# Kernel optimization log

Hardware: AMD Instinct MI355X
Metric: run time of the kernel (lower is better)

The kernel has to match this reference:

```python
import jax, jax.numpy as jnp
import numpy as np

# Fixed inverse-Haar 2x2 filters (spatial only; depth kernel size is 1)
K_LL = jnp.array([[0.5, 0.5], [0.5, 0.5]], dtype=jnp.float32)
K_LH = jnp.array([[-0.5, 0.5], [-0.5, 0.5]], dtype=jnp.float32)
K_HL = jnp.array([[-0.5, -0.5], [0.5, 0.5]], dtype=jnp.float32)
K_HH = jnp.array([[0.5, -0.5], [-0.5, 0.5]], dtype=jnp.float32)


def _upsample2x(v, k):
    # conv_transpose3d with single-channel 1x2x2 kernel, stride (1,2,2):
    # out[b,d,2i+p,2j+q] = v[b,d,i,j] * k[p,q]
    b, d, h, w = v.shape
    o = jnp.einsum('bdhw,pq->bdhpwq', v, k)
    return o.reshape(b, d, 2 * h, 2 * w)


def setup_inputs() -> dict:
    key = jax.random.key(0)
    k1, k2, k3 = jax.random.split(key, 3)
    B, D, H, W = 8, 32, 128, 128
    x_LL = jax.random.normal(k1, (B, D, H, W), dtype=jnp.float32)
    x = jax.random.normal(k2, (B, 4, D, H, W), dtype=jnp.float32)
    y = jax.random.normal(k3, (B, D, 2 * H, 2 * W), dtype=jnp.float32)
    return {"x_LL": x_LL, "x": x, "y": y}


def reference(x_LL, x, y):
    LL = _upsample2x(x_LL, K_LL)
    LH = _upsample2x(x[:, 1], K_LH)
    HL = _upsample2x(x[:, 2], K_HL)
    HH = _upsample2x(x[:, 3], K_HH)
    return jnp.concatenate((LL, LH, HL, HH, y), axis=1)
```

## Files before the change

kernel.cpp:

```cpp
#include <hip/hip_runtime.h>


#define BB 8
#define DD 32
#define HH_IN 128
#define WW_IN 128
#define H2 256
#define W2 256
#define C_OUT 160
#define W4 64

__global__ __launch_bounds__(256) void haar_iwt_cat_kernel(
    const float* __restrict__ xLL,
    const float* __restrict__ x,
    const float* __restrict__ y,
    float*       __restrict__ out,
    long long total4)
{
    const long long stride = (long long)gridDim.x * blockDim.x;
    for (long long idx = (long long)blockIdx.x * blockDim.x + threadIdx.x;
         idx < total4; idx += stride) {
        const int w4       = (int)(idx & (W4 - 1));
        const long long t1 = idx >> 6;
        const int h2       = (int)(t1 & (H2 - 1));
        const long long bc = t1 >> 8;
        const int c        = (int)(bc % C_OUT);
        const int b        = (int)(bc / C_OUT);

        float4 o;
        if (c >= 128) {
            const int d = c - 128;
            const float4* src = (const float4*)(
                y + ((((long long)b * DD + d) * H2 + h2) * (long long)W2));
            o = src[w4];
        } else {
            const int sel = c >> 5;
            const int d   = c & 31;
            const int h   = h2 >> 1;
            const int p   = h2 & 1;
            const float* src;
            if (sel == 0) {
                src = xLL + ((((long long)b * DD + d) * HH_IN + h) * (long long)WW_IN);
            } else {
                src = x + (((((long long)b * 4 + sel) * DD + d) * HH_IN + h) * (long long)WW_IN);
            }
            const float2 v = ((const float2*)src)[w4];
            float k0, k1;
            switch (sel) {
                case 0:  k0 =  0.5f;              k1 =  0.5f; break;
                case 1:  k0 = -0.5f;              k1 =  0.5f; break;
                case 2:  k0 = p ?  0.5f : -0.5f;  k1 =  k0;   break;
                default: k0 = p ? -0.5f :  0.5f;  k1 = -k0;   break;
            }
            o.x = v.x * k0;
            o.y = v.x * k1;
            o.z = v.y * k0;
            o.w = v.y * k1;
        }
        ((float4*)out)[idx] = o;
    }
}

extern "C" void kernel_launch(void* const* d_in, const int* in_sizes, int n_in,
                              void* d_out, int out_size, void* d_ws, size_t ws_size,
                              hipStream_t stream) {
    const float* xLL = (const float*)d_in[0];
    const float* x   = (const float*)d_in[1];
    const float* y   = (const float*)d_in[2];
    float*       out = (float*)d_out;

    const long long total4 = (long long)BB * C_OUT * H2 * W4;
    const int block = 256;
    const int grid  = 2048;

    haar_iwt_cat_kernel<<<grid, block, 0, stream>>>(xLL, x, y, out, total4);
}
```

Measured before the change: 94.95 us.

## Map each wavefront to one input row, emitting two output rows with nontemporal accesses

After: 85.95 us. 1.1x faster.

```diff
diff --git a/kernel.cpp b/kernel.cpp
--- a/kernel.cpp
+++ b/kernel.cpp
@@ -1,64 +1,63 @@
 #include <hip/hip_runtime.h>
 
 
-#define BB 8
 #define DD 32
-#define HH_IN 128
-#define WW_IN 128
+#define H_IN 128
+#define W_IN 128
 #define H2 256
 #define W2 256
-#define C_OUT 160
-#define W4 64
+
+typedef float f32x4 __attribute__((ext_vector_type(4)));
+typedef float f32x2 __attribute__((ext_vector_type(2)));
 
 __global__ __launch_bounds__(256) void haar_iwt_cat_kernel(
     const float* __restrict__ xLL,
     const float* __restrict__ x,
     const float* __restrict__ y,
-    float*       __restrict__ out,
-    long long total4)
+    float*       __restrict__ out)
 {
-    const long long stride = (long long)gridDim.x * blockDim.x;
-    for (long long idx = (long long)blockIdx.x * blockDim.x + threadIdx.x;
-         idx < total4; idx += stride) {
-        const int w4       = (int)(idx & (W4 - 1));
-        const long long t1 = idx >> 6;
-        const int h2       = (int)(t1 & (H2 - 1));
-        const long long bc = t1 >> 8;
-        const int c        = (int)(bc % C_OUT);
-        const int b        = (int)(bc / C_OUT);
+    const unsigned tid  = threadIdx.x;
+    const unsigned lane = tid & 63u;
+    const unsigned u = blockIdx.x * 4u + (tid >> 6);
 
-        float4 o;
-        if (c >= 128) {
-            const int d = c - 128;
-            const float4* src = (const float4*)(
-                y + ((((long long)b * DD + d) * H2 + h2) * (long long)W2));
-            o = src[w4];
-        } else {
-            const int sel = c >> 5;
-            const int d   = c & 31;
-            const int h   = h2 >> 1;
-            const int p   = h2 & 1;
-            const float* src;
-            if (sel == 0) {
-                src = xLL + ((((long long)b * DD + d) * HH_IN + h) * (long long)WW_IN);
-            } else {
-                src = x + (((((long long)b * 4 + sel) * DD + d) * HH_IN + h) * (long long)WW_IN);
-            }
-            const float2 v = ((const float2*)src)[w4];
-            float k0, k1;
-            switch (sel) {
-                case 0:  k0 =  0.5f;              k1 =  0.5f; break;
-                case 1:  k0 = -0.5f;              k1 =  0.5f; break;
-                case 2:  k0 = p ?  0.5f : -0.5f;  k1 =  k0;   break;
-                default: k0 = p ? -0.5f :  0.5f;  k1 = -k0;   break;
-            }
-            o.x = v.x * k0;
-            o.y = v.x * k1;
-            o.z = v.y * k0;
-            o.w = v.y * k1;
-        }
-        ((float4*)out)[idx] = o;
+    const unsigned i = u & (H_IN - 1u);
+    unsigned t = u >> 7;
+    const unsigned d = t & (DD - 1u);
+    t >>= 5;
+    const unsigned b   = t / 5u;
+    const unsigned sel = t - b * 5u;
+
+    float* orow = out + (((size_t)(b * 160u + sel * 32u + d) * H2 + 2u * i) * W2);
+    f32x4* o0 = ((f32x4*)orow) + lane;
+    f32x4* o1 = ((f32x4*)(orow + W2)) + lane;
+
+    if (sel == 4u) {
+        const float* yrow = y + (((size_t)(b * DD + d) * H2 + 2u * i) * W2);
+        const f32x4 v0 = __builtin_nontemporal_load(((const f32x4*)yrow) + lane);
+        const f32x4 v1 = __builtin_nontemporal_load(((const f32x4*)(yrow + W2)) + lane);
+        __builtin_nontemporal_store(v0, o0);
+        __builtin_nontemporal_store(v1, o1);
+        return;
     }
+
+    const float* src = (sel == 0u)
+        ? xLL + ((size_t)(b * DD + d) * H_IN + i) * W_IN
+        : x   + ((size_t)((b * 4u + sel) * DD + d) * H_IN + i) * W_IN;
+    const f32x2 v = __builtin_nontemporal_load(((const f32x2*)src) + lane);
+
+    float k00, k01, k10, k11;
+    switch (sel) {
+        case 0u: k00 =  0.5f; k01 =  0.5f; k10 =  0.5f; k11 =  0.5f; break;
+        case 1u: k00 = -0.5f; k01 =  0.5f; k10 = -0.5f; k11 =  0.5f; break;
+        case 2u: k00 = -0.5f; k01 = -0.5f; k10 =  0.5f; k11 =  0.5f; break;
+        default: k00 =  0.5f; k01 = -0.5f; k10 = -0.5f; k11 =  0.5f; break;
+    }
+
+    f32x4 r0, r1;
+    r0.x = v.x * k00; r0.y = v.x * k01; r0.z = v.y * k00; r0.w = v.y * k01;
+    r1.x = v.x * k10; r1.y = v.x * k11; r1.z = v.y * k10; r1.w = v.y * k11;
+    __builtin_nontemporal_store(r0, o0);
+    __builtin_nontemporal_store(r1, o1);
 }
 
 extern "C" void kernel_launch(void* const* d_in, const int* in_sizes, int n_in,
@@ -69,9 +68,7 @@
     const float* y   = (const float*)d_in[2];
     float*       out = (float*)d_out;
 
-    const long long total4 = (long long)BB * C_OUT * H2 * W4;
+    const int grid  = 163840 / 4;
     const int block = 256;
-    const int grid  = 2048;
-
-    haar_iwt_cat_kernel<<<grid, block, 0, stream>>>(xLL, x, y, out, total4);
+    haar_iwt_cat_kernel<<<grid, block, 0, stream>>>(xLL, x, y, out);
 }
```
